# Kernel optimization log

Measured on AMD Instinct MI355X. Metric: run time of the kernel, lower is better.

The kernel has to match this reference:

```python
import jax, jax.numpy as jnp
import numpy as np

H = 768
I = 3072
E = 8
B, S = 2, 512
EPS = 1e-12


def setup_inputs() -> dict:
    key = jax.random.key(0)
    ks = jax.random.split(key, 8)
    hidden_states = jax.random.normal(ks[0], (B, S, H), dtype=jnp.float32)
    expert_idx = jax.random.randint(ks[1], (B * S,), 0, E)
    scale1 = 1.0 / np.sqrt(H)
    scale2 = 1.0 / np.sqrt(I)
    W1 = jax.random.uniform(ks[2], (E, H, I), jnp.float32, -scale1, scale1)
    b1 = jax.random.uniform(ks[3], (E, I), jnp.float32, -scale1, scale1)
    W2 = jax.random.uniform(ks[4], (E, I, H), jnp.float32, -scale2, scale2)
    b2 = jax.random.uniform(ks[5], (E, H), jnp.float32, -scale2, scale2)
    gamma = jnp.ones((H,), jnp.float32)
    beta = jnp.zeros((H,), jnp.float32)
    return {
        "hidden_states": hidden_states,
        "expert_idx": expert_idx,
        "W1": W1, "b1": b1, "W2": W2, "b2": b2,
        "gamma": gamma, "beta": beta,
    }


def _moe_ln(hidden_states, expert_idx, W1, b1, W2, b2, gamma, beta):
    b, s, h = hidden_states.shape
    x = hidden_states.reshape(-1, h)  # [T, H]
    out = jnp.zeros_like(x)
    # loop over the small fixed expert count; select per-token results by mask
    for e in range(E):
        inter = jax.nn.gelu(x @ W1[e] + b1[e], approximate=False)
        y_e = inter @ W2[e] + b2[e]
        out = jnp.where((expert_idx == e)[:, None], y_e, out)
    y = out.reshape(b, s, h) + hidden_states  # residual
    mu = jnp.mean(y, axis=-1, keepdims=True)
    var = jnp.mean(jnp.square(y - mu), axis=-1, keepdims=True)
    return (y - mu) * jax.lax.rsqrt(var + EPS) * gamma + beta


def reference(hidden_states, expert_idx, W1, b1, W2, b2, gamma, beta):
    return _moe_ln(hidden_states, expert_idx, W1, b1, W2, b2, gamma, beta)
```

## Files before the change

kernel.cpp:

```cpp
#include <hip/hip_runtime.h>
#include <math.h>

#define T_TOK 1024
#define H_DIM 768
#define I_DIM 3072
#define E_NUM 8
#define BM    128
#define BN    64
#define BK    64
#define MSLOTS 16
#define KSPLIT2 4
#define CONV_Y 16
#define NCONVB (48 * CONV_Y)
#define CONV_CHUNKS (E_NUM * I_DIM * H_DIM / 8)
#define CONV_PER_T (CONV_CHUNKS / (NCONVB * 512))
#define CVT_BLKS 2304
#define GATHER_BLKS (T_TOK * (H_DIM / 8) / 512)

typedef __attribute__((ext_vector_type(8))) short  short8;
typedef __attribute__((ext_vector_type(4))) float  f32x4;

__device__ __forceinline__ unsigned short f2bf(float f) {
  union { float f; unsigned u; } a; a.f = f;
  unsigned r = a.u + 0x7FFFu + ((a.u >> 16) & 1u);
  return (unsigned short)(r >> 16);
}
__device__ __forceinline__ float gelu_exact(float x) {
  return 0.5f * x * (1.0f + erff(x * 0.70710678118654752f));
}
__device__ __forceinline__ int swz(int row, int k) {
  return row * BK + (k ^ ((row & 7) << 3));
}
__device__ __forceinline__ void gll16(const void* g, void* l) {
  __builtin_amdgcn_global_load_lds(
      (const __attribute__((address_space(1))) void*)g,
      (__attribute__((address_space(3))) void*)l, 16, 0, 0);
}
__device__ __forceinline__ short8 cvt8(const float4 a, const float4 b) {
  short8 o;
  o[0] = (short)f2bf(a.x); o[1] = (short)f2bf(a.y);
  o[2] = (short)f2bf(a.z); o[3] = (short)f2bf(a.w);
  o[4] = (short)f2bf(b.x); o[5] = (short)f2bf(b.y);
  o[6] = (short)f2bf(b.z); o[7] = (short)f2bf(b.w);
  return o;
}

__global__ __launch_bounds__(1024) void route_kernel(
    const int* __restrict__ eidx, int* __restrict__ perm,
    int* __restrict__ tile_e, int* __restrict__ tile_row,
    int* __restrict__ tile_len, int* __restrict__ ntiles) {
  __shared__ int wcnt[16][E_NUM];
  __shared__ int wpre[16][E_NUM];
  __shared__ int offsh[E_NUM + 1];
  const int t = threadIdx.x;
  const int lane = t & 63, wave = t >> 6;
  const int e = eidx[t];
  unsigned long long myMask = 0;
#pragma unroll
  for (int ee = 0; ee < E_NUM; ++ee) {
    unsigned long long m = __ballot(e == ee);
    if (ee == e) myMask = m;
    if (lane == 0) wcnt[wave][ee] = __popcll(m);
  }
  const int rank = __popcll(myMask & ((1ull << lane) - 1ull));
  __syncthreads();
  if (t < 16 * E_NUM) {
    const int w = t >> 3, ee = t & 7;
    int p = 0;
    for (int w2 = 0; w2 < w; ++w2) p += wcnt[w2][ee];
    wpre[w][ee] = p;
  }
  __syncthreads();
  if (t <= E_NUM) {
    int off = 0;
    for (int ee = 0; ee < t; ++ee) off += wpre[15][ee] + wcnt[15][ee];
    offsh[t] = off;
  }
  __syncthreads();
  perm[offsh[e] + wpre[wave][e] + rank] = t;
  if (t == 0) {
    int n = 0;
    for (int ee = 0; ee < E_NUM; ++ee)
      for (int r = offsh[ee]; r < offsh[ee + 1]; r += BM) {
        tile_e[n] = ee; tile_row[n] = r;
        tile_len[n] = min(offsh[ee + 1] - r, BM); ++n;
      }
    *ntiles = n;
    for (int i = n; i < MSLOTS; ++i) { tile_e[i] = 0; tile_row[i] = 0; tile_len[i] = 0; }
  }
}

__global__ __launch_bounds__(512) void gather_cvt_kernel(
    const float* __restrict__ x, const int* __restrict__ perm,
    unsigned short* __restrict__ xg,
    const float* __restrict__ W1, unsigned short* __restrict__ w1b, int nCvt) {
  const int b = blockIdx.x;
  const int t = threadIdx.x;
  if (b < nCvt) {
    const float4* s4 = (const float4*)W1;
    short8* d8 = (short8*)w1b;
#pragma unroll
    for (int j = 0; j < 2; ++j) {
      const int idx = j * (CVT_BLKS * 512) + b * 512 + t;
      d8[idx] = cvt8(s4[2 * idx], s4[2 * idx + 1]);
    }
    return;
  }
  const int idx = (b - nCvt) * 512 + t;
  const int p = idx / (H_DIM / 8);
  const int c = (idx % (H_DIM / 8)) * 8;
  const int tok = perm[p];
  const float* src = x + (size_t)tok * H_DIM + c;
  *(short8*)(xg + (size_t)p * H_DIM + c) =
      cvt8(*(const float4*)(src), *(const float4*)(src + 4));
}

template <int N_FULL, int K_FULL, int KLOOP, bool IS_FFN1, bool B_BF16>
__global__ __launch_bounds__(512, 4) void moe_gemm(
    const unsigned short* __restrict__ A,
    const void* __restrict__ Wv,
    const float* __restrict__ bias,
    const int* __restrict__ tile_e, const int* __restrict__ tile_row,
    const int* __restrict__ tile_len, const int* __restrict__ ntiles,
    unsigned short* __restrict__ out_bf,
    float* __restrict__ part,
    const float* __restrict__ convSrc,
    unsigned short* __restrict__ convDst) {
  constexpr int KT = KLOOP / BK;
  const int tid  = threadIdx.x;
  int slot = blockIdx.y;

  if constexpr (IS_FFN1 && B_BF16) {
    if (slot < CONV_Y) {
      const int cb  = blockIdx.x + 48 * slot;
      const float4* s4 = (const float4*)convSrc;
      short8* d8 = (short8*)convDst;
#pragma unroll
      for (int j = 0; j < CONV_PER_T; ++j) {
        const int idx = j * (NCONVB * 512) + cb * 512 + tid;
        d8[idx] = cvt8(s4[2 * idx], s4[2 * idx + 1]);
      }
      return;
    }
    slot -= CONV_Y;
  }
  if (slot >= *ntiles) return;
  const int e    = tile_e[slot];
  const int row0 = tile_row[slot];
  const int len  = tile_len[slot];
  const int n0   = blockIdx.x * BN;
  const int kbase = blockIdx.z * KLOOP;

  __shared__ unsigned short As[2][BM * BK];
  __shared__ unsigned short Bs[2][BN * BK];

  const int lane = tid & 63;
  const int wave = tid >> 6;
  const int wm = wave >> 1, wn = wave & 1;
  const int lr = lane & 15;
  const int lk = (lane >> 4) * 8;

  const unsigned short* agsrc[2];
  int aoff[2];
#pragma unroll
  for (int i = 0; i < 2; ++i) {
    const int c = tid + i * 512;
    const int r = c >> 3, kc = (c & 7) << 3;
    int grow = row0 + r; grow = grow < T_TOK ? grow : (T_TOK - 1);
    agsrc[i] = A + (size_t)grow * K_FULL + kbase + (kc ^ ((r & 7) << 3));
    aoff[i]  = ((tid & ~63) + i * 512) * 8;
  }
  const int bn_ = tid & 63;
  const int kb8 = (tid >> 6) * 8;
  const float* wpF = nullptr; const unsigned short* wpH = nullptr;
  if constexpr (B_BF16)
    wpH = (const unsigned short*)Wv + (size_t)e * K_FULL * N_FULL +
          (size_t)(kbase + kb8) * N_FULL + n0 + bn_;
  else
    wpF = (const float*)Wv + (size_t)e * K_FULL * N_FULL +
          (size_t)(kbase + kb8) * N_FULL + n0 + bn_;

  f32x4 acc[2][2] = {};
  float Xf[8], Yf[8];
  unsigned short Xh[8], Yh[8];

  auto issueA = [&](int kt, int buf) {
#pragma unroll
    for (int i = 0; i < 2; ++i)
      gll16(agsrc[i] + kt * BK, &As[buf][aoff[i]]);
  };
  auto loadB = [&](int kt, float* df, unsigned short* dh) {
#pragma unroll
    for (int j = 0; j < 8; ++j) {
      if constexpr (B_BF16) dh[j] = wpH[(size_t)(kt * BK + j) * N_FULL];
      else                  df[j] = wpF[(size_t)(kt * BK + j) * N_FULL];
    }
  };
  auto writeB = [&](int buf, const float* df, const unsigned short* dh) {
    short8 p;
#pragma unroll
    for (int j = 0; j < 8; ++j)
      p[j] = B_BF16 ? (short)dh[j] : (short)f2bf(df[j]);
    *(short8*)(&Bs[buf][swz(bn_, kb8)]) = p;
  };
  auto mfma_tile = [&](int buf) {
#pragma unroll
    for (int ks = 0; ks < 2; ++ks) {
      const int kp = ks * 32 + lk;
      short8 af[2], bfr[2];
#pragma unroll
      for (int m = 0; m < 2; ++m)
        af[m] = *(const short8*)(&As[buf][swz(wm * 32 + m * 16 + lr, kp)]);
#pragma unroll
      for (int n = 0; n < 2; ++n)
        bfr[n] = *(const short8*)(&Bs[buf][swz(wn * 32 + n * 16 + lr, kp)]);
#pragma unroll
      for (int m = 0; m < 2; ++m)
#pragma unroll
        for (int n = 0; n < 2; ++n)
          acc[m][n] = __builtin_amdgcn_mfma_f32_16x16x32_bf16(af[m], bfr[n], acc[m][n], 0, 0, 0);
    }
  };
  auto phase = [&](int t, int buf, float* cf, unsigned short* ch,
                   bool nextA, bool nextB, bool drain) {
    if (drain) asm volatile("s_waitcnt vmcnt(0)" ::: "memory");
    else       asm volatile("s_waitcnt vmcnt(8)" ::: "memory");
    writeB(buf, cf, ch);
    asm volatile("s_waitcnt lgkmcnt(0)" ::: "memory");
    __builtin_amdgcn_s_barrier();
    __builtin_amdgcn_sched_barrier(0);
    if (nextA) issueA(t + 1, buf ^ 1);
    __builtin_amdgcn_sched_barrier(0);
    if (nextB) loadB(t + 2, cf, ch);
    __builtin_amdgcn_sched_barrier(0);
    mfma_tile(buf);
  };

  loadB(0, Xf, Xh);
  __builtin_amdgcn_sched_barrier(0);
  issueA(0, 0);
  __builtin_amdgcn_sched_barrier(0);
  loadB(1, Yf, Yh);
#pragma unroll 1
  for (int t = 0; t < KT - 2; t += 2) {
    phase(t,     0, Xf, Xh, true, true, false);
    phase(t + 1, 1, Yf, Yh, true, true, false);
  }
  phase(KT - 2, 0, Xf, Xh, true,  false, false);
  phase(KT - 1, 1, Yf, Yh, false, false, true);

#pragma unroll
  for (int n = 0; n < 2; ++n) {
    const int gc = n0 + wn * 32 + n * 16 + lr;
    float bv = 0.f;
    if constexpr (IS_FFN1) bv = bias[(size_t)e * N_FULL + gc];
#pragma unroll
    for (int m = 0; m < 2; ++m) {
      const int rbase = wm * 32 + m * 16 + (lane >> 4) * 4;
#pragma unroll
      for (int j = 0; j < 4; ++j) {
        const int rl = rbase + j;
        if (rl < len) {
          if constexpr (IS_FFN1) {
            out_bf[(size_t)(row0 + rl) * N_FULL + gc] = f2bf(gelu_exact(acc[m][n][j] + bv));
          } else {
            part[((size_t)blockIdx.z * T_TOK + row0 + rl) * N_FULL + gc] = acc[m][n][j];
          }
        }
      }
    }
  }
}

__global__ void ln_kernel(const float* __restrict__ part,
                          const float* __restrict__ x,
                          const int* __restrict__ perm,
                          const int* __restrict__ eidx,
                          const float* __restrict__ b2,
                          const float* __restrict__ gamma,
                          const float* __restrict__ beta,
                          float* __restrict__ out) {
  const int p = blockIdx.x;
  const int tid = threadIdx.x;
  const int t = perm[p];
  const int e = eidx[t];
  float v[3], s = 0.f, ss = 0.f;
#pragma unroll
  for (int i = 0; i < 3; ++i) {
    const int c = tid + i * 256;
    float a = x[(size_t)t * H_DIM + c] + b2[(size_t)e * H_DIM + c];
#pragma unroll
    for (int s4 = 0; s4 < KSPLIT2; ++s4)
      a += part[((size_t)s4 * T_TOK + p) * H_DIM + c];
    v[i] = a; s += a; ss += a * a;
  }
#pragma unroll
  for (int o = 32; o; o >>= 1) { s += __shfl_down(s, o); ss += __shfl_down(ss, o); }
  __shared__ float ps[4], pss[4];
  __shared__ float mu_s, ir_s;
  const int w = tid >> 6;
  if ((tid & 63) == 0) { ps[w] = s; pss[w] = ss; }
  __syncthreads();
  if (tid == 0) {
    const float S = ps[0] + ps[1] + ps[2] + ps[3];
    const float SS = pss[0] + pss[1] + pss[2] + pss[3];
    const float mu = S * (1.0f / H_DIM);
    const float var = SS * (1.0f / H_DIM) - mu * mu;
    mu_s = mu; ir_s = rsqrtf(var + 1e-12f);
  }
  __syncthreads();
  const float mu = mu_s, ir = ir_s;
#pragma unroll
  for (int i = 0; i < 3; ++i) {
    const int c = tid + i * 256;
    out[(size_t)t * H_DIM + c] = (v[i] - mu) * ir * gamma[c] + beta[c];
  }
}

extern "C" void kernel_launch(void* const* d_in, const int* in_sizes, int n_in,
                              void* d_out, int out_size, void* d_ws, size_t ws_size,
                              hipStream_t stream) {
  const float* x     = (const float*)d_in[0];
  const int*   eidx  = (const int*)d_in[1];
  const float* W1    = (const float*)d_in[2];
  const float* b1    = (const float*)d_in[3];
  const float* W2    = (const float*)d_in[4];
  const float* b2    = (const float*)d_in[5];
  const float* gamma = (const float*)d_in[6];
  const float* beta  = (const float*)d_in[7];
  float* out = (float*)d_out;

  char* ws = (char*)d_ws;
  int* perm     = (int*)(ws);
  int* tile_e   = (int*)(ws + 4096);
  int* tile_row = (int*)(ws + 4352);
  int* tile_len = (int*)(ws + 4608);
  int* ntiles   = (int*)(ws + 4864);
  size_t off = 8192;
  unsigned short* xg = (unsigned short*)(ws + off);    off += (size_t)2 * T_TOK * H_DIM;
  unsigned short* inter = (unsigned short*)(ws + off); off += (size_t)2 * T_TOK * I_DIM;
  float* part = (float*)(ws + off);                    off += (size_t)4 * KSPLIT2 * T_TOK * H_DIM;
  unsigned short* w1b = (unsigned short*)(ws + off);   off += (size_t)2 * E_NUM * H_DIM * I_DIM;
  unsigned short* w2b = (unsigned short*)(ws + off);
  const size_t need = off + (size_t)2 * E_NUM * H_DIM * I_DIM;
  const bool bf = ws_size >= need;

  route_kernel<<<1, T_TOK, 0, stream>>>(eidx, perm, tile_e, tile_row, tile_len, ntiles);
  if (bf) {
    gather_cvt_kernel<<<CVT_BLKS + GATHER_BLKS, 512, 0, stream>>>(
        x, perm, xg, W1, w1b, CVT_BLKS);
    moe_gemm<I_DIM, H_DIM, H_DIM, true, true>
        <<<dim3(I_DIM / BN, CONV_Y + MSLOTS, 1), 512, 0, stream>>>(
        xg, w1b, b1, tile_e, tile_row, tile_len, ntiles, inter, nullptr, W2, w2b);
    moe_gemm<H_DIM, I_DIM, I_DIM / KSPLIT2, false, true>
        <<<dim3(H_DIM / BN, MSLOTS, KSPLIT2), 512, 0, stream>>>(
        inter, w2b, nullptr, tile_e, tile_row, tile_len, ntiles, nullptr, part,
        nullptr, nullptr);
  } else {
    gather_cvt_kernel<<<GATHER_BLKS, 512, 0, stream>>>(x, perm, xg, nullptr, nullptr, 0);
    moe_gemm<I_DIM, H_DIM, H_DIM, true, false>
        <<<dim3(I_DIM / BN, MSLOTS, 1), 512, 0, stream>>>(
        xg, W1, b1, tile_e, tile_row, tile_len, ntiles, inter, nullptr,
        nullptr, nullptr);
    moe_gemm<H_DIM, I_DIM, I_DIM / KSPLIT2, false, false>
        <<<dim3(H_DIM / BN, MSLOTS, KSPLIT2), 512, 0, stream>>>(
        inter, W2, nullptr, tile_e, tile_row, tile_len, ntiles, nullptr, part,
        nullptr, nullptr);
  }
  ln_kernel<<<T_TOK, 256, 0, stream>>>(part, x, perm, eidx, b2, gamma, beta, out);
  (void)in_sizes; (void)n_in; (void)out_size;
}
```

Measured before the change: 91.29 us.

## Split weight conversion into dedicated kernel and pad W1 bf16 row stride

Moves the fp32-to-bf16 conversion of both W1 and W2 into one standalone conversion kernel, replacing the old scheme that overlapped W1 conversion with the gather and W2 conversion with the FFN1 GEMM. The bf16 W1 copy is stored with a padded row stride of 3200 elements, meant to avoid cache or channel conflicts from the power-of-two stride on strided B loads. This gives up the previous overlap of conversion with other work in exchange for simpler launches and a better-behaved W1 stride. It adds a serial full-weight conversion pass before the first GEMM.

After: 96.60 us. 1.06x slower.

```diff
diff --git a/kernel.cpp b/kernel.cpp
--- a/kernel.cpp
+++ b/kernel.cpp
@@ -10,11 +10,11 @@
 #define BK    64
 #define MSLOTS 16
 #define KSPLIT2 4
-#define CONV_Y 16
-#define NCONVB (48 * CONV_Y)
-#define CONV_CHUNKS (E_NUM * I_DIM * H_DIM / 8)
-#define CONV_PER_T (CONV_CHUNKS / (NCONVB * 512))
-#define CVT_BLKS 2304
+#define LDB1  3200
+#define W1_CHUNKS (E_NUM * H_DIM * I_DIM / 8)
+#define W2_CHUNKS (E_NUM * I_DIM * H_DIM / 8)
+#define CVT_PER_T 4
+#define CVT_BLOCKS ((W1_CHUNKS + W2_CHUNKS) / (512 * CVT_PER_T))
 #define GATHER_BLKS (T_TOK * (H_DIM / 8) / 512)
 
 typedef __attribute__((ext_vector_type(8))) short  short8;
@@ -90,23 +90,10 @@
   }
 }
 
-__global__ __launch_bounds__(512) void gather_cvt_kernel(
+__global__ __launch_bounds__(512) void gather_kernel(
     const float* __restrict__ x, const int* __restrict__ perm,
-    unsigned short* __restrict__ xg,
-    const float* __restrict__ W1, unsigned short* __restrict__ w1b, int nCvt) {
-  const int b = blockIdx.x;
-  const int t = threadIdx.x;
-  if (b < nCvt) {
-    const float4* s4 = (const float4*)W1;
-    short8* d8 = (short8*)w1b;
-#pragma unroll
-    for (int j = 0; j < 2; ++j) {
-      const int idx = j * (CVT_BLKS * 512) + b * 512 + t;
-      d8[idx] = cvt8(s4[2 * idx], s4[2 * idx + 1]);
-    }
-    return;
-  }
-  const int idx = (b - nCvt) * 512 + t;
+    unsigned short* __restrict__ xg) {
+  const int idx = blockIdx.x * 512 + threadIdx.x;
   const int p = idx / (H_DIM / 8);
   const int c = (idx % (H_DIM / 8)) * 8;
   const int tok = perm[p];
@@ -115,7 +102,29 @@
       cvt8(*(const float4*)(src), *(const float4*)(src + 4));
 }
 
-template <int N_FULL, int K_FULL, int KLOOP, bool IS_FFN1, bool B_BF16>
+__global__ __launch_bounds__(512) void cvt_kernel(
+    const float* __restrict__ W1, unsigned short* __restrict__ w1b,
+    const float* __restrict__ W2, unsigned short* __restrict__ w2b) {
+  const int base = blockIdx.x * 512 + threadIdx.x;
+#pragma unroll
+  for (int j = 0; j < CVT_PER_T; ++j) {
+    const int idx = j * (CVT_BLOCKS * 512) + base;
+    if (idx < W1_CHUNKS) {
+      const float4 a = ((const float4*)W1)[2 * idx];
+      const float4 b = ((const float4*)W1)[2 * idx + 1];
+      const int r = idx / (I_DIM / 8);
+      const int c = (idx % (I_DIM / 8)) * 8;
+      *(short8*)(w1b + (size_t)r * LDB1 + c) = cvt8(a, b);
+    } else {
+      const int k = idx - W1_CHUNKS;
+      const float4 a = ((const float4*)W2)[2 * k];
+      const float4 b = ((const float4*)W2)[2 * k + 1];
+      ((short8*)w2b)[k] = cvt8(a, b);
+    }
+  }
+}
+
+template <int N_FULL, int K_FULL, int KLOOP, int LDB, bool IS_FFN1, bool B_BF16>
 __global__ __launch_bounds__(512, 4) void moe_gemm(
     const unsigned short* __restrict__ A,
     const void* __restrict__ Wv,
@@ -123,27 +132,10 @@
     const int* __restrict__ tile_e, const int* __restrict__ tile_row,
     const int* __restrict__ tile_len, const int* __restrict__ ntiles,
     unsigned short* __restrict__ out_bf,
-    float* __restrict__ part,
-    const float* __restrict__ convSrc,
-    unsigned short* __restrict__ convDst) {
+    float* __restrict__ part) {
   constexpr int KT = KLOOP / BK;
   const int tid  = threadIdx.x;
-  int slot = blockIdx.y;
-
-  if constexpr (IS_FFN1 && B_BF16) {
-    if (slot < CONV_Y) {
-      const int cb  = blockIdx.x + 48 * slot;
-      const float4* s4 = (const float4*)convSrc;
-      short8* d8 = (short8*)convDst;
-#pragma unroll
-      for (int j = 0; j < CONV_PER_T; ++j) {
-        const int idx = j * (NCONVB * 512) + cb * 512 + tid;
-        d8[idx] = cvt8(s4[2 * idx], s4[2 * idx + 1]);
-      }
-      return;
-    }
-    slot -= CONV_Y;
-  }
+  const int slot = blockIdx.y;
   if (slot >= *ntiles) return;
   const int e    = tile_e[slot];
   const int row0 = tile_row[slot];
@@ -174,8 +166,8 @@
   const int kb8 = (tid >> 6) * 8;
   const float* wpF = nullptr; const unsigned short* wpH = nullptr;
   if constexpr (B_BF16)
-    wpH = (const unsigned short*)Wv + (size_t)e * K_FULL * N_FULL +
-          (size_t)(kbase + kb8) * N_FULL + n0 + bn_;
+    wpH = (const unsigned short*)Wv + (size_t)e * K_FULL * LDB +
+          (size_t)(kbase + kb8) * LDB + n0 + bn_;
   else
     wpF = (const float*)Wv + (size_t)e * K_FULL * N_FULL +
           (size_t)(kbase + kb8) * N_FULL + n0 + bn_;
@@ -192,7 +184,7 @@
   auto loadB = [&](int kt, float* df, unsigned short* dh) {
 #pragma unroll
     for (int j = 0; j < 8; ++j) {
-      if constexpr (B_BF16) dh[j] = wpH[(size_t)(kt * BK + j) * N_FULL];
+      if constexpr (B_BF16) dh[j] = wpH[(size_t)(kt * BK + j) * LDB];
       else                  df[j] = wpF[(size_t)(kt * BK + j) * N_FULL];
     }
   };
@@ -340,32 +332,28 @@
   unsigned short* xg = (unsigned short*)(ws + off);    off += (size_t)2 * T_TOK * H_DIM;
   unsigned short* inter = (unsigned short*)(ws + off); off += (size_t)2 * T_TOK * I_DIM;
   float* part = (float*)(ws + off);                    off += (size_t)4 * KSPLIT2 * T_TOK * H_DIM;
-  unsigned short* w1b = (unsigned short*)(ws + off);   off += (size_t)2 * E_NUM * H_DIM * I_DIM;
+  unsigned short* w1b = (unsigned short*)(ws + off);   off += (size_t)2 * E_NUM * H_DIM * LDB1;
   unsigned short* w2b = (unsigned short*)(ws + off);
-  const size_t need = off + (size_t)2 * E_NUM * H_DIM * I_DIM;
+  const size_t need = off + (size_t)2 * E_NUM * I_DIM * H_DIM;
   const bool bf = ws_size >= need;
 
   route_kernel<<<1, T_TOK, 0, stream>>>(eidx, perm, tile_e, tile_row, tile_len, ntiles);
+  gather_kernel<<<GATHER_BLKS, 512, 0, stream>>>(x, perm, xg);
   if (bf) {
-    gather_cvt_kernel<<<CVT_BLKS + GATHER_BLKS, 512, 0, stream>>>(
-        x, perm, xg, W1, w1b, CVT_BLKS);
-    moe_gemm<I_DIM, H_DIM, H_DIM, true, true>
-        <<<dim3(I_DIM / BN, CONV_Y + MSLOTS, 1), 512, 0, stream>>>(
-        xg, w1b, b1, tile_e, tile_row, tile_len, ntiles, inter, nullptr, W2, w2b);
-    moe_gemm<H_DIM, I_DIM, I_DIM / KSPLIT2, false, true>
+    cvt_kernel<<<CVT_BLOCKS, 512, 0, stream>>>(W1, w1b, W2, w2b);
+    moe_gemm<I_DIM, H_DIM, H_DIM, LDB1, true, true>
+        <<<dim3(I_DIM / BN, MSLOTS, 1), 512, 0, stream>>>(
+        xg, w1b, b1, tile_e, tile_row, tile_len, ntiles, inter, nullptr);
+    moe_gemm<H_DIM, I_DIM, I_DIM / KSPLIT2, H_DIM, false, true>
         <<<dim3(H_DIM / BN, MSLOTS, KSPLIT2), 512, 0, stream>>>(
-        inter, w2b, nullptr, tile_e, tile_row, tile_len, ntiles, nullptr, part,
-        nullptr, nullptr);
+        inter, w2b, nullptr, tile_e, tile_row, tile_len, ntiles, nullptr, part);
   } else {
-    gather_cvt_kernel<<<GATHER_BLKS, 512, 0, stream>>>(x, perm, xg, nullptr, nullptr, 0);
-    moe_gemm<I_DIM, H_DIM, H_DIM, true, false>
+    moe_gemm<I_DIM, H_DIM, H_DIM, I_DIM, true, false>
         <<<dim3(I_DIM / BN, MSLOTS, 1), 512, 0, stream>>>(
-        xg, W1, b1, tile_e, tile_row, tile_len, ntiles, inter, nullptr,
-        nullptr, nullptr);
-    moe_gemm<H_DIM, I_DIM, I_DIM / KSPLIT2, false, false>
+        xg, W1, b1, tile_e, tile_row, tile_len, ntiles, inter, nullptr);
+    moe_gemm<H_DIM, I_DIM, I_DIM / KSPLIT2, H_DIM, false, false>
         <<<dim3(H_DIM / BN, MSLOTS, KSPLIT2), 512, 0, stream>>>(
-        inter, W2, nullptr, tile_e, tile_row, tile_len, ntiles, nullptr, part,
-        nullptr, nullptr);
+        inter, W2, nullptr, tile_e, tile_row, tile_len, ntiles, nullptr, part);
   }
   ln_kernel<<<T_TOK, 256, 0, stream>>>(part, x, perm, eidx, b2, gamma, beta, out);
   (void)in_sizes; (void)n_in; (void)out_size;
```
